# Optimization experiments

Measured on AMD Instinct MI355X. Metric: run time of the kernel, lower is better.

Reference implementation:

```python
import jax, jax.numpy as jnp
import numpy as np

B, N, F_IN, F_OUT, E = 2, 8192, 64, 64, 262144
ALPHA = 0.2  # LeakyReLU negative slope


def setup_inputs() -> dict:
    key = jax.random.key(0)
    k1, k2, k3, k4, k5 = jax.random.split(key, 5)
    h = jax.random.normal(k1, (B, N, F_IN), dtype=jnp.float32)
    edge_index = jax.random.randint(k2, (2, E), 0, N, dtype=jnp.int64)
    edge_weight = jax.random.uniform(k3, (E,), dtype=jnp.float32)
    # torch Linear(in,out,bias=False): weight shape (out, in)
    lim_w = float(np.sqrt(1.0 / F_IN))
    W = jax.random.uniform(k4, (F_OUT, F_IN), minval=-lim_w, maxval=lim_w, dtype=jnp.float32)
    # xavier_uniform on (2*out, 1)
    lim_a = float(np.sqrt(6.0 / (2 * F_OUT + 1)))
    a = jax.random.uniform(k5, (2 * F_OUT, 1), minval=-lim_a, maxval=lim_a, dtype=jnp.float32)
    return {"h": h, "W": W, "a": a, "edge_index": edge_index, "edge_weight": edge_weight}


def reference(h, W, a, edge_index, edge_weight):
    src, dst = edge_index[0], edge_index[1]

    def single(hb):  # hb: (N, F_IN)
        Wh = hb @ W.T  # (N, F_OUT)
        edge_h = jnp.concatenate([Wh[src], Wh[dst]], axis=1)  # (E, 2*F_OUT)
        e = jax.nn.leaky_relu((edge_h @ a)[:, 0], negative_slope=ALPHA)  # (E,)
        e = e * edge_weight
        # dense N x N attention, zeros treated as masked (faithful to source)
        attn = jnp.zeros((N, N), dtype=Wh.dtype).at[src, dst].set(e)
        mask = attn == 0
        attn = jnp.where(mask, -jnp.inf, attn)
        attn = jax.nn.softmax(attn, axis=1)
        attn = jnp.where(mask, 0.0, attn)
        h_prime = attn @ Wh  # (N, F_OUT)
        return jax.nn.elu(h_prime)  # concat=True path

    return jax.vmap(single)(h)
```

## Files before the change

kernel.cpp:

```cpp
#include <hip/hip_runtime.h>
#include <hip/hip_bf16.h>
#include <math.h>

#define NN     8192
#define FDIM   64
#define EDGES  262144
#define BATCH  2
#define ALPHA  0.2f

#define NB     256
#define SRCB   32
#define BCAP   1280
#define ROWCAP 128

#define OFF_WH    0u
#define OFF_S1    4194304u
#define OFF_S2    4259840u
#define OFF_OFFS  4325376u
#define OFF_CRS   4456448u
#define OFF_CEW   6553600u

__global__ __launch_bounds__(1024) void stage1_kernel(
    const float* __restrict__ h, const float* __restrict__ W,
    const float* __restrict__ a, const int* __restrict__ ei,
    const float* __restrict__ ew,
    float* __restrict__ Wh, float* __restrict__ s1g, float* __restrict__ s2g,
    unsigned short* __restrict__ offsT, uint2* __restrict__ coarse,
    float* __restrict__ cew) {
  __shared__ float sW[64 * 65];
  __shared__ float sH[64 * 64];
  __shared__ int hist[NB];
  __shared__ int offs[NB];
  int tid = threadIdx.x, lane = tid & 63, w = tid >> 6;
  int blk = blockIdx.x;

  int e = blk * 1024 + tid;
  int s = ei[e], d = ei[EDGES + e];
  int g = s >> 5;
  if (tid < NB) hist[tid] = 0;
  __syncthreads();
  int rank = atomicAdd(&hist[g], 1);
  __syncthreads();
  if (tid < 64) {
    int i0 = tid * 4;
    int c0 = hist[i0], c1 = hist[i0 + 1], c2 = hist[i0 + 2], c3 = hist[i0 + 3];
    int sum = c0 + c1 + c2 + c3;
    int x = sum;
#pragma unroll
    for (int off = 1; off < 64; off <<= 1) {
      int y = __shfl_up(x, off, 64);
      if (tid >= off) x += y;
    }
    int ex = x - sum;
    offs[i0] = ex; offs[i0 + 1] = ex + c0;
    offs[i0 + 2] = ex + c0 + c1; offs[i0 + 3] = ex + c0 + c1 + c2;
  }
  __syncthreads();
  float wgt = ew[e];
  int pos = blk * 1024 + offs[g] + rank;
  coarse[pos] = make_uint2(((unsigned)e << 13) | (unsigned)d, (unsigned)s);
  cew[pos] = wgt;
  if (tid < NB) offsT[tid * 256 + blk] = (unsigned short)offs[tid];

  for (int i = tid; i < 4096; i += 1024) sW[(i >> 6) * 65 + (i & 63)] = W[i];
  int rr = lane >> 4, c4 = lane & 15;
  int nn0 = blk * 64 + w * 4;
  *(float4*)(sH + (w * 4 + rr) * 64 + c4 * 4) =
      *(const float4*)(h + (size_t)(nn0 + rr) * 64 + c4 * 4);
  __syncthreads();

  const float* wp = sW + lane * 65;
  const float* hp = sH + (w * 4) * 64;
  float acc[4] = {0.f, 0.f, 0.f, 0.f};
#pragma unroll 8
  for (int k = 0; k < 64; ++k) {
    float wv = wp[k];
    acc[0] += hp[k] * wv;
    acc[1] += hp[64 + k] * wv;
    acc[2] += hp[128 + k] * wv;
    acc[3] += hp[192 + k] * wv;
  }
  float a1 = a[lane], a2 = a[64 + lane];
#pragma unroll
  for (int r = 0; r < 4; ++r) {
    int nn = nn0 + r;
    Wh[(size_t)nn * 64 + lane] = acc[r];
    float p1 = acc[r] * a1, p2 = acc[r] * a2;
#pragma unroll
    for (int off = 32; off; off >>= 1) {
      p1 += __shfl_xor(p1, off, 64);
      p2 += __shfl_xor(p2, off, 64);
    }
    if (lane == 0) { s1g[nn] = p1; s2g[nn] = p2; }
  }
}

__global__ __launch_bounds__(1024) void stage2_kernel(
    const float* __restrict__ s1g, const float* __restrict__ s2g,
    const unsigned short* __restrict__ offsT, const uint2* __restrict__ coarse,
    const float* __restrict__ cew, const float* __restrict__ Wh,
    float* __restrict__ out) {
  __shared__ uint2 grp[BCAP];
  __shared__ int dstBase[257];
  __shared__ int srcPos[256];
  __shared__ int rhist[SRCB];
  __shared__ int roffs[SRCB];
  __shared__ float s1loc[SRCB];
  __shared__ unsigned bmap[16 * 256];
  int tid = threadIdx.x, lane = tid & 63, w = tid >> 6;
  int blk = blockIdx.x;
  int xcd = blk & 7;
  int b = xcd >> 2;
  int g = (blk >> 3) * 4 + (xcd & 3);
  const float* s2b = s2g + b * NN;
  if (tid < SRCB) {
    rhist[tid] = 0;
    s1loc[tid] = s1g[b * NN + g * SRCB + tid];
  }

  if (tid < 256) {
    int lo = offsT[g * 256 + tid];
    int hi = (g == 255) ? 1024 : offsT[(g + 1) * 256 + tid];
    srcPos[tid] = tid * 1024 + lo;
    dstBase[tid] = hi - lo;
  }
  __syncthreads();
  if (tid < 64) {
    int i0 = tid * 4;
    int c0 = dstBase[i0], c1 = dstBase[i0 + 1], c2 = dstBase[i0 + 2], c3 = dstBase[i0 + 3];
    int sum = c0 + c1 + c2 + c3;
    int x = sum;
#pragma unroll
    for (int off = 1; off < 64; off <<= 1) {
      int y = __shfl_up(x, off, 64);
      if (tid >= off) x += y;
    }
    int ex = x - sum;
    dstBase[i0] = ex; dstBase[i0 + 1] = ex + c0;
    dstBase[i0 + 2] = ex + c0 + c1; dstBase[i0 + 3] = ex + c0 + c1 + c2;
    if (tid == 63) dstBase[256] = x;
  }
  __syncthreads();
  int T = dstBase[256]; if (T > BCAP) T = BCAP;

  unsigned mpk[2]; float mv[2]; int msl[2], mrk[2]; bool mok[2];
#pragma unroll
  for (int j = 0; j < 2; ++j) {
    int i = tid + j * 1024;
    mok[j] = (i < T);
    mpk[j] = 0; mv[j] = 0.f; msl[j] = 0; mrk[j] = 0;
    if (mok[j]) {
      int lo = 0, hi = 255;
#pragma unroll
      for (int st = 0; st < 8; ++st) {
        int mid = (lo + hi + 1) >> 1;
        if (dstBase[mid] <= i) lo = mid; else hi = mid - 1;
      }
      int c = lo, jj = i - dstBase[c];
      uint2 E = coarse[srcPos[c] + jj];
      float wgt = cew[srcPos[c] + jj];
      int dst = (int)(E.x & 0x1FFFu);
      int src = (int)E.y;
      float x = s1loc[src & (SRCB - 1)] + s2b[dst];
      float val = (x > 0.f ? x : ALPHA * x) * wgt;
      mpk[j] = E.x; mv[j] = val; msl[j] = src & (SRCB - 1);
      mrk[j] = atomicAdd(&rhist[msl[j]], 1);
    }
  }
  __syncthreads();
  if (tid < SRCB) {
    int c = rhist[tid];
    int x = c;
#pragma unroll
    for (int off = 1; off < SRCB; off <<= 1) {
      int y = __shfl_up(x, off, 64);
      if (tid >= off) x += y;
    }
    roffs[tid] = x - c;
  }
  __syncthreads();
#pragma unroll
  for (int j = 0; j < 2; ++j)
    if (mok[j]) grp[roffs[msl[j]] + mrk[j]] = make_uint2(mpk[j], __float_as_uint(mv[j]));
  __syncthreads();

  const float* Whb = Wh + (size_t)b * NN * FDIM;
  unsigned* mywords = bmap + w * 256;
  int fg = lane & 15, es = lane >> 4;
  for (int q = 0; q < 2; ++q) {
    int slo = w * 2 + q;
    int beg = roffs[slo];
    int deg = rhist[slo];
    int n = g * SRCB + slo;
    float4 r4 = make_float4(0.f, 0.f, 0.f, 0.f);
    if (deg > 0) {
      float inv;
      if (deg <= 64) {
        unsigned k0 = 0; float v0 = 0.f;
        if (lane < deg) { uint2 E = grp[beg + lane]; k0 = E.x; v0 = __uint_as_float(E.y); }
#pragma unroll
        for (int u = 0; u < 4; ++u) mywords[u * 64 + lane] = 0u;
        bool dup = false;
        if (lane < deg) {
          int dst = (int)(k0 & 0x1FFFu);
          unsigned old = atomicOr(&mywords[dst >> 5], 1u << (dst & 31));
          dup = (old >> (dst & 31)) & 1u;
        }
        if (__ballot(dup) != 0ull) {
          for (int j = 0; j < deg; ++j) {
            unsigned q2 = __shfl(k0, j, 64);
            if ((((q2 ^ k0) & 0x1FFFu) == 0u) & (q2 > k0)) v0 = 0.f;
          }
        }
        float m = (v0 != 0.f) ? v0 : -INFINITY;
#pragma unroll
        for (int off = 32; off; off >>= 1) m = fmaxf(m, __shfl_xor(m, off, 64));
        float p = (v0 != 0.f) ? expf(v0 - m) : 0.f;
        float sum = p;
#pragma unroll
        for (int off = 32; off; off >>= 1) sum += __shfl_xor(sum, off, 64);
        inv = (sum > 0.f) ? 1.f / sum : 0.f;
        if (lane < deg) grp[beg + lane].y = __float_as_uint(p);
      } else {
        int dg = deg > ROWCAP ? ROWCAP : deg;
        deg = dg;
        unsigned k0 = 0, k1 = 0; float v0 = 0.f, v1 = 0.f;
        { uint2 E = grp[beg + lane]; k0 = E.x; v0 = __uint_as_float(E.y); }
        if (lane + 64 < dg) { uint2 E = grp[beg + lane + 64]; k1 = E.x; v1 = __uint_as_float(E.y); }
        for (int j = 0; j < 64; ++j) {
          unsigned q2 = __shfl(k0, j, 64);
          if ((((q2 ^ k0) & 0x1FFFu) == 0u) & (q2 > k0)) v0 = 0.f;
          if ((((q2 ^ k1) & 0x1FFFu) == 0u) & (q2 > k1)) v1 = 0.f;
        }
        for (int j = 0; j < dg - 64; ++j) {
          unsigned q2 = __shfl(k1, j, 64);
          if ((((q2 ^ k0) & 0x1FFFu) == 0u) & (q2 > k0)) v0 = 0.f;
          if ((((q2 ^ k1) & 0x1FFFu) == 0u) & (q2 > k1)) v1 = 0.f;
        }
        float m = fmaxf((v0 != 0.f) ? v0 : -INFINITY, (v1 != 0.f) ? v1 : -INFINITY);
#pragma unroll
        for (int off = 32; off; off >>= 1) m = fmaxf(m, __shfl_xor(m, off, 64));
        float p0 = (v0 != 0.f) ? expf(v0 - m) : 0.f;
        float p1 = (v1 != 0.f) ? expf(v1 - m) : 0.f;
        float sum = p0 + p1;
#pragma unroll
        for (int off = 32; off; off >>= 1) sum += __shfl_xor(sum, off, 64);
        inv = (sum > 0.f) ? 1.f / sum : 0.f;
        grp[beg + lane].y = __float_as_uint(p0);
        if (lane + 64 < dg) grp[beg + lane + 64].y = __float_as_uint(p1);
      }
      float4 acc = make_float4(0.f, 0.f, 0.f, 0.f);
      for (int kk = 0; kk < deg; kk += 32) {
        float4 vv[8]; float pp[8];
#pragma unroll
        for (int u = 0; u < 8; ++u) {
          int k = kk + u * 4 + es;
          int kc = k < deg ? k : deg - 1;
          uint2 E = grp[beg + kc];
          pp[u] = (k < deg) ? __uint_as_float(E.y) : 0.f;
          vv[u] = *((const float4*)(Whb + (E.x & 0x1FFFu) * 64) + fg);
        }
#pragma unroll
        for (int u = 0; u < 8; ++u) {
          acc.x += pp[u] * vv[u].x; acc.y += pp[u] * vv[u].y;
          acc.z += pp[u] * vv[u].z; acc.w += pp[u] * vv[u].w;
        }
      }
#pragma unroll
      for (int off = 16; off <= 32; off <<= 1) {
        acc.x += __shfl_xor(acc.x, off, 64);
        acc.y += __shfl_xor(acc.y, off, 64);
        acc.z += __shfl_xor(acc.z, off, 64);
        acc.w += __shfl_xor(acc.w, off, 64);
      }
      r4.x = acc.x * inv; r4.y = acc.y * inv; r4.z = acc.z * inv; r4.w = acc.w * inv;
    }
    if (es == 0) {
      r4.x = r4.x > 0.f ? r4.x : expm1f(r4.x);
      r4.y = r4.y > 0.f ? r4.y : expm1f(r4.y);
      r4.z = r4.z > 0.f ? r4.z : expm1f(r4.z);
      r4.w = r4.w > 0.f ? r4.w : expm1f(r4.w);
      *((float4*)(out + ((size_t)b * NN + n) * 64) + fg) = r4;
    }
  }
}

extern "C" void kernel_launch(void* const* d_in, const int* in_sizes, int n_in,
                              void* d_out, int out_size, void* d_ws, size_t ws_size,
                              hipStream_t stream) {
  const float* h  = (const float*)d_in[0];
  const float* W  = (const float*)d_in[1];
  const float* a  = (const float*)d_in[2];
  const int*   ei = (const int*)d_in[3];
  const float* ew = (const float*)d_in[4];
  float* out = (float*)d_out;

  char* ws = (char*)d_ws;
  float*          Wh     = (float*)(ws + OFF_WH);
  float*          s1     = (float*)(ws + OFF_S1);
  float*          s2     = (float*)(ws + OFF_S2);
  unsigned short* offsT  = (unsigned short*)(ws + OFF_OFFS);
  uint2*          coarse = (uint2*)(ws + OFF_CRS);
  float*          cew    = (float*)(ws + OFF_CEW);

  stage1_kernel<<<256, 1024, 0, stream>>>(h, W, a, ei, ew, Wh, s1, s2, offsT, coarse, cew);
  stage2_kernel<<<BATCH * NB, 1024, 0, stream>>>(s1, s2, offsT, coarse, cew, Wh, out);
}
```

Before: 101.0 us.

## Replace two-level counting sort with global atomic per-row edge buckets

Stage 1 no longer does a per-block histogram and prefix sum. Instead each edge atomically claims a slot in a fixed-capacity per-source-row bucket in global memory, with counters padded to spread contention. Stage 2 reads each row's edges directly, with no gather through prefix sums, binary search or LDS regrouping, and computes the attention logits per row inside the wave. It adds a memset launch and global atomics, and the edge order within a row is now nondeterministic, though duplicates are resolved by edge-id comparison.

```diff
diff --git a/kernel.cpp b/kernel.cpp
--- a/kernel.cpp
+++ b/kernel.cpp
@@ -1,5 +1,4 @@
 #include <hip/hip_runtime.h>
-#include <hip/hip_bf16.h>
 #include <math.h>
 
 #define NN     8192
@@ -8,59 +7,29 @@
 #define BATCH  2
 #define ALPHA  0.2f
 
-#define NB     256
-#define SRCB   32
-#define BCAP   1280
 #define ROWCAP 128
+#define CNTPAD 16
 
 #define OFF_WH    0u
 #define OFF_S1    4194304u
 #define OFF_S2    4259840u
-#define OFF_OFFS  4325376u
-#define OFF_CRS   4456448u
-#define OFF_CEW   6553600u
+#define OFF_CNT   4325376u
+#define OFF_ROWS  4849664u
 
 __global__ __launch_bounds__(1024) void stage1_kernel(
     const float* __restrict__ h, const float* __restrict__ W,
     const float* __restrict__ a, const int* __restrict__ ei,
     const float* __restrict__ ew,
     float* __restrict__ Wh, float* __restrict__ s1g, float* __restrict__ s2g,
-    unsigned short* __restrict__ offsT, uint2* __restrict__ coarse,
-    float* __restrict__ cew) {
+    int* __restrict__ cnt, uint2* __restrict__ rows) {
   __shared__ float sW[64 * 65];
   __shared__ float sH[64 * 64];
-  __shared__ int hist[NB];
-  __shared__ int offs[NB];
   int tid = threadIdx.x, lane = tid & 63, w = tid >> 6;
   int blk = blockIdx.x;
 
   int e = blk * 1024 + tid;
   int s = ei[e], d = ei[EDGES + e];
-  int g = s >> 5;
-  if (tid < NB) hist[tid] = 0;
-  __syncthreads();
-  int rank = atomicAdd(&hist[g], 1);
-  __syncthreads();
-  if (tid < 64) {
-    int i0 = tid * 4;
-    int c0 = hist[i0], c1 = hist[i0 + 1], c2 = hist[i0 + 2], c3 = hist[i0 + 3];
-    int sum = c0 + c1 + c2 + c3;
-    int x = sum;
-#pragma unroll
-    for (int off = 1; off < 64; off <<= 1) {
-      int y = __shfl_up(x, off, 64);
-      if (tid >= off) x += y;
-    }
-    int ex = x - sum;
-    offs[i0] = ex; offs[i0 + 1] = ex + c0;
-    offs[i0 + 2] = ex + c0 + c1; offs[i0 + 3] = ex + c0 + c1 + c2;
-  }
-  __syncthreads();
   float wgt = ew[e];
-  int pos = blk * 1024 + offs[g] + rank;
-  coarse[pos] = make_uint2(((unsigned)e << 13) | (unsigned)d, (unsigned)s);
-  cew[pos] = wgt;
-  if (tid < NB) offsT[tid * 256 + blk] = (unsigned short)offs[tid];
 
   for (int i = tid; i < 4096; i += 1024) sW[(i >> 6) * 65 + (i & 63)] = W[i];
   int rr = lane >> 4, c4 = lane & 15;
@@ -93,111 +62,59 @@
     }
     if (lane == 0) { s1g[nn] = p1; s2g[nn] = p2; }
   }
+
+  int rank = atomicAdd(&cnt[s * CNTPAD], 1);
+  if (rank < ROWCAP)
+    rows[s * ROWCAP + rank] =
+        make_uint2(((unsigned)e << 13) | (unsigned)d, __float_as_uint(wgt));
 }
 
 __global__ __launch_bounds__(1024) void stage2_kernel(
     const float* __restrict__ s1g, const float* __restrict__ s2g,
-    const unsigned short* __restrict__ offsT, const uint2* __restrict__ coarse,
-    const float* __restrict__ cew, const float* __restrict__ Wh,
-    float* __restrict__ out) {
-  __shared__ uint2 grp[BCAP];
-  __shared__ int dstBase[257];
-  __shared__ int srcPos[256];
-  __shared__ int rhist[SRCB];
-  __shared__ int roffs[SRCB];
-  __shared__ float s1loc[SRCB];
+    const int* __restrict__ cnt, const uint2* __restrict__ rows,
+    const float* __restrict__ Wh, float* __restrict__ out) {
   __shared__ unsigned bmap[16 * 256];
+  __shared__ uint2 sE[16 * ROWCAP];
   int tid = threadIdx.x, lane = tid & 63, w = tid >> 6;
   int blk = blockIdx.x;
   int xcd = blk & 7;
   int b = xcd >> 2;
   int g = (blk >> 3) * 4 + (xcd & 3);
   const float* s2b = s2g + b * NN;
-  if (tid < SRCB) {
-    rhist[tid] = 0;
-    s1loc[tid] = s1g[b * NN + g * SRCB + tid];
-  }
-
-  if (tid < 256) {
-    int lo = offsT[g * 256 + tid];
-    int hi = (g == 255) ? 1024 : offsT[(g + 1) * 256 + tid];
-    srcPos[tid] = tid * 1024 + lo;
-    dstBase[tid] = hi - lo;
-  }
-  __syncthreads();
-  if (tid < 64) {
-    int i0 = tid * 4;
-    int c0 = dstBase[i0], c1 = dstBase[i0 + 1], c2 = dstBase[i0 + 2], c3 = dstBase[i0 + 3];
-    int sum = c0 + c1 + c2 + c3;
-    int x = sum;
-#pragma unroll
-    for (int off = 1; off < 64; off <<= 1) {
-      int y = __shfl_up(x, off, 64);
-      if (tid >= off) x += y;
-    }
-    int ex = x - sum;
-    dstBase[i0] = ex; dstBase[i0 + 1] = ex + c0;
-    dstBase[i0 + 2] = ex + c0 + c1; dstBase[i0 + 3] = ex + c0 + c1 + c2;
-    if (tid == 63) dstBase[256] = x;
-  }
-  __syncthreads();
-  int T = dstBase[256]; if (T > BCAP) T = BCAP;
-
-  unsigned mpk[2]; float mv[2]; int msl[2], mrk[2]; bool mok[2];
-#pragma unroll
-  for (int j = 0; j < 2; ++j) {
-    int i = tid + j * 1024;
-    mok[j] = (i < T);
-    mpk[j] = 0; mv[j] = 0.f; msl[j] = 0; mrk[j] = 0;
-    if (mok[j]) {
-      int lo = 0, hi = 255;
-#pragma unroll
-      for (int st = 0; st < 8; ++st) {
-        int mid = (lo + hi + 1) >> 1;
-        if (dstBase[mid] <= i) lo = mid; else hi = mid - 1;
-      }
-      int c = lo, jj = i - dstBase[c];
-      uint2 E = coarse[srcPos[c] + jj];
-      float wgt = cew[srcPos[c] + jj];
-      int dst = (int)(E.x & 0x1FFFu);
-      int src = (int)E.y;
-      float x = s1loc[src & (SRCB - 1)] + s2b[dst];
-      float val = (x > 0.f ? x : ALPHA * x) * wgt;
-      mpk[j] = E.x; mv[j] = val; msl[j] = src & (SRCB - 1);
-      mrk[j] = atomicAdd(&rhist[msl[j]], 1);
-    }
-  }
-  __syncthreads();
-  if (tid < SRCB) {
-    int c = rhist[tid];
-    int x = c;
-#pragma unroll
-    for (int off = 1; off < SRCB; off <<= 1) {
-      int y = __shfl_up(x, off, 64);
-      if (tid >= off) x += y;
-    }
-    roffs[tid] = x - c;
-  }
-  __syncthreads();
-#pragma unroll
-  for (int j = 0; j < 2; ++j)
-    if (mok[j]) grp[roffs[msl[j]] + mrk[j]] = make_uint2(mpk[j], __float_as_uint(mv[j]));
-  __syncthreads();
-
   const float* Whb = Wh + (size_t)b * NN * FDIM;
   unsigned* mywords = bmap + w * 256;
+  uint2* myE = sE + w * ROWCAP;
   int fg = lane & 15, es = lane >> 4;
+
   for (int q = 0; q < 2; ++q) {
-    int slo = w * 2 + q;
-    int beg = roffs[slo];
-    int deg = rhist[slo];
-    int n = g * SRCB + slo;
+    int n = g * 32 + w * 2 + q;
+    int deg = cnt[n * CNTPAD];
+    if (deg > ROWCAP) deg = ROWCAP;
     float4 r4 = make_float4(0.f, 0.f, 0.f, 0.f);
     if (deg > 0) {
-      float inv;
-      if (deg <= 64) {
-        unsigned k0 = 0; float v0 = 0.f;
-        if (lane < deg) { uint2 E = grp[beg + lane]; k0 = E.x; v0 = __uint_as_float(E.y); }
+      float s1v = s1g[b * NN + n];
+      bool two = deg > 64;
+      unsigned k0 = 0, k1 = 0; float w0 = 0.f, w1 = 0.f;
+      if (lane < deg) {
+        uint2 E = rows[n * ROWCAP + lane];
+        k0 = E.x; w0 = __uint_as_float(E.y);
+      }
+      if (two && lane + 64 < deg) {
+        uint2 E = rows[n * ROWCAP + 64 + lane];
+        k1 = E.x; w1 = __uint_as_float(E.y);
+      }
+      float v0 = 0.f, v1 = 0.f;
+      if (lane < deg) {
+        int dst = (int)(k0 & 0x1FFFu);
+        float x = s1v + s2b[dst];
+        v0 = (x > 0.f ? x : ALPHA * x) * w0;
+      }
+      if (two && lane + 64 < deg) {
+        int dst = (int)(k1 & 0x1FFFu);
+        float x = s1v + s2b[dst];
+        v1 = (x > 0.f ? x : ALPHA * x) * w1;
+      }
+      if (!two) {
 #pragma unroll
         for (int u = 0; u < 4; ++u) mywords[u * 64 + lane] = 0u;
         bool dup = false;
@@ -212,43 +129,31 @@
             if ((((q2 ^ k0) & 0x1FFFu) == 0u) & (q2 > k0)) v0 = 0.f;
           }
         }
-        float m = (v0 != 0.f) ? v0 : -INFINITY;
-#pragma unroll
-        for (int off = 32; off; off >>= 1) m = fmaxf(m, __shfl_xor(m, off, 64));
-        float p = (v0 != 0.f) ? expf(v0 - m) : 0.f;
-        float sum = p;
-#pragma unroll
-        for (int off = 32; off; off >>= 1) sum += __shfl_xor(sum, off, 64);
-        inv = (sum > 0.f) ? 1.f / sum : 0.f;
-        if (lane < deg) grp[beg + lane].y = __float_as_uint(p);
       } else {
-        int dg = deg > ROWCAP ? ROWCAP : deg;
-        deg = dg;
-        unsigned k0 = 0, k1 = 0; float v0 = 0.f, v1 = 0.f;
-        { uint2 E = grp[beg + lane]; k0 = E.x; v0 = __uint_as_float(E.y); }
-        if (lane + 64 < dg) { uint2 E = grp[beg + lane + 64]; k1 = E.x; v1 = __uint_as_float(E.y); }
         for (int j = 0; j < 64; ++j) {
           unsigned q2 = __shfl(k0, j, 64);
           if ((((q2 ^ k0) & 0x1FFFu) == 0u) & (q2 > k0)) v0 = 0.f;
           if ((((q2 ^ k1) & 0x1FFFu) == 0u) & (q2 > k1)) v1 = 0.f;
         }
-        for (int j = 0; j < dg - 64; ++j) {
+        for (int j = 0; j < deg - 64; ++j) {
           unsigned q2 = __shfl(k1, j, 64);
           if ((((q2 ^ k0) & 0x1FFFu) == 0u) & (q2 > k0)) v0 = 0.f;
           if ((((q2 ^ k1) & 0x1FFFu) == 0u) & (q2 > k1)) v1 = 0.f;
         }
-        float m = fmaxf((v0 != 0.f) ? v0 : -INFINITY, (v1 != 0.f) ? v1 : -INFINITY);
-#pragma unroll
-        for (int off = 32; off; off >>= 1) m = fmaxf(m, __shfl_xor(m, off, 64));
-        float p0 = (v0 != 0.f) ? expf(v0 - m) : 0.f;
-        float p1 = (v1 != 0.f) ? expf(v1 - m) : 0.f;
-        float sum = p0 + p1;
-#pragma unroll
-        for (int off = 32; off; off >>= 1) sum += __shfl_xor(sum, off, 64);
-        inv = (sum > 0.f) ? 1.f / sum : 0.f;
-        grp[beg + lane].y = __float_as_uint(p0);
-        if (lane + 64 < dg) grp[beg + lane + 64].y = __float_as_uint(p1);
-      }
+      }
+      float m = fmaxf((v0 != 0.f) ? v0 : -INFINITY,
+                      (two && v1 != 0.f) ? v1 : -INFINITY);
+#pragma unroll
+      for (int off = 32; off; off >>= 1) m = fmaxf(m, __shfl_xor(m, off, 64));
+      float p0 = (v0 != 0.f) ? expf(v0 - m) : 0.f;
+      float p1 = (two && v1 != 0.f) ? expf(v1 - m) : 0.f;
+      float sum = p0 + p1;
+#pragma unroll
+      for (int off = 32; off; off >>= 1) sum += __shfl_xor(sum, off, 64);
+      float inv = (sum > 0.f) ? 1.f / sum : 0.f;
+      if (lane < deg) myE[lane] = make_uint2(k0 & 0x1FFFu, __float_as_uint(p0));
+      if (two && lane + 64 < deg)
+        myE[64 + lane] = make_uint2(k1 & 0x1FFFu, __float_as_uint(p1));
       float4 acc = make_float4(0.f, 0.f, 0.f, 0.f);
       for (int kk = 0; kk < deg; kk += 32) {
         float4 vv[8]; float pp[8];
@@ -256,9 +161,9 @@
         for (int u = 0; u < 8; ++u) {
           int k = kk + u * 4 + es;
           int kc = k < deg ? k : deg - 1;
-          uint2 E = grp[beg + kc];
+          uint2 E = myE[kc];
           pp[u] = (k < deg) ? __uint_as_float(E.y) : 0.f;
-          vv[u] = *((const float4*)(Whb + (E.x & 0x1FFFu) * 64) + fg);
+          vv[u] = *((const float4*)(Whb + (size_t)E.x * 64) + fg);
         }
 #pragma unroll
         for (int u = 0; u < 8; ++u) {
@@ -296,13 +201,13 @@
   float* out = (float*)d_out;
 
   char* ws = (char*)d_ws;
-  float*          Wh     = (float*)(ws + OFF_WH);
-  float*          s1     = (float*)(ws + OFF_S1);
-  float*          s2     = (float*)(ws + OFF_S2);
-  unsigned short* offsT  = (unsigned short*)(ws + OFF_OFFS);
-  uint2*          coarse = (uint2*)(ws + OFF_CRS);
-  float*          cew    = (float*)(ws + OFF_CEW);
-
-  stage1_kernel<<<256, 1024, 0, stream>>>(h, W, a, ei, ew, Wh, s1, s2, offsT, coarse, cew);
-  stage2_kernel<<<BATCH * NB, 1024, 0, stream>>>(s1, s2, offsT, coarse, cew, Wh, out);
+  float* Wh   = (float*)(ws + OFF_WH);
+  float* s1   = (float*)(ws + OFF_S1);
+  float* s2   = (float*)(ws + OFF_S2);
+  int*   cnt  = (int*)(ws + OFF_CNT);
+  uint2* rows = (uint2*)(ws + OFF_ROWS);
+
+  hipMemsetAsync(cnt, 0, NN * CNTPAD * sizeof(int), stream);
+  stage1_kernel<<<256, 1024, 0, stream>>>(h, W, a, ei, ew, Wh, s1, s2, cnt, rows);
+  stage2_kernel<<<BATCH * 256, 1024, 0, stream>>>(s1, s2, cnt, rows, Wh, out);
 }
```

Result: slower. 106.7 us (+5.7%).
